# Optimization experiments

Hardware: AMD Instinct MI355X
Metric: run time of the kernel (lower is better)

Reference implementation:

```python
import jax, jax.numpy as jnp
import numpy as np
from jax import lax


def conv2d(x, w, pad):
    return lax.conv_general_dilated(x, w, (1, 1), [(pad, pad), (pad, pad)],
                                    dimension_numbers=('NCHW', 'OIHW', 'NCHW'))


def deform_conv2d(x, offset, w, b, k, pad):
    # torchvision-style DeformConv2d, stride 1, dilation 1, 1 group.
    # offset: [B, 2*k*k, H, W], pairs ordered (dy, dx) per kernel tap (row-major).
    B, C, H, W = x.shape
    KK = k * k
    off = offset.reshape(B, KK, 2, H, W)
    ky, kx = jnp.meshgrid(jnp.arange(k), jnp.arange(k), indexing='ij')
    ky = ky.reshape(1, KK, 1, 1).astype(x.dtype)
    kx = kx.reshape(1, KK, 1, 1).astype(x.dtype)
    gy = jnp.arange(H, dtype=x.dtype).reshape(1, 1, H, 1)
    gx = jnp.arange(W, dtype=x.dtype).reshape(1, 1, 1, W)
    ys = gy + ky - pad + off[:, :, 0]  # [B, KK, H, W]
    xs = gx + kx - pad + off[:, :, 1]
    y0 = jnp.floor(ys)
    x0 = jnp.floor(xs)
    y1 = y0 + 1.0
    x1 = x0 + 1.0
    img = x.reshape(B, C, H * W)

    def corner(yc, xc, wt):
        # zero padding outside the image
        valid = (yc >= 0) & (yc <= H - 1) & (xc >= 0) & (xc <= W - 1)
        idx = (jnp.clip(yc, 0, H - 1) * W + jnp.clip(xc, 0, W - 1)).astype(jnp.int32).reshape(B, -1)
        g = jax.vmap(lambda im, ix: jnp.take(im, ix, axis=1))(img, idx)  # [B, C, KK*H*W]
        return g.reshape(B, C, KK, H, W) * (wt * valid)[:, None]

    v = (corner(y0, x0, (y1 - ys) * (x1 - xs))
         + corner(y0, x1, (y1 - ys) * (xs - x0))
         + corner(y1, x0, (ys - y0) * (x1 - xs))
         + corner(y1, x1, (ys - y0) * (xs - x0)))  # [B, C, KK, H, W]
    out = jnp.einsum('bckhw,ock->bohw', v, w.reshape(w.shape[0], C, KK))
    return out + b[None, :, None, None]


def setup_inputs() -> dict:
    key = jax.random.key(0)
    ks = jax.random.split(key, 16)
    f32 = jnp.float32
    dim = 64

    def rn(k, shape, s):
        return jax.random.normal(k, shape, f32) * s

    return {
        'x': rn(ks[0], (4, dim, 96, 96), 1.0),
        'w_off3': rn(ks[1], (18, dim, 3, 3), 0.01), 'b_off3': jnp.zeros((18,), f32),
        'w_off5': rn(ks[2], (50, dim, 3, 3), 0.01), 'b_off5': jnp.zeros((50,), f32),
        'w_off7': rn(ks[3], (98, dim, 3, 3), 0.01), 'b_off7': jnp.zeros((98,), f32),
        'w_d3': rn(ks[4], (dim, dim, 3, 3), 0.04), 'b_d3': rn(ks[5], (dim,), 0.01),
        'w_d5': rn(ks[6], (dim, dim, 5, 5), 0.025), 'b_d5': rn(ks[7], (dim,), 0.01),
        'w_d7': rn(ks[8], (dim, dim, 7, 7), 0.018), 'b_d7': rn(ks[9], (dim,), 0.01),
        'w_sp': rn(ks[10], (1, 2, 7, 7), 0.1),
        'w_ca1': rn(ks[11], (12, 3 * dim, 1, 1), 0.07),
        'w_ca2': rn(ks[12], (3 * dim, 12, 1, 1), 0.28),
    }


def reference(x, w_off3, b_off3, w_off5, b_off5, w_off7, b_off7,
              w_d3, b_d3, w_d5, b_d5, w_d7, b_d7, w_sp, w_ca1, w_ca2):
    off3 = conv2d(x, w_off3, 1) + b_off3[None, :, None, None]
    off5 = conv2d(x, w_off5, 1) + b_off5[None, :, None, None]
    off7 = conv2d(x, w_off7, 1) + b_off7[None, :, None, None]
    a1 = deform_conv2d(x, off3, w_d3, b_d3, 3, 1)
    a2 = deform_conv2d(x, off5, w_d5, b_d5, 5, 2)
    a3 = deform_conv2d(x, off7, w_d7, b_d7, 7, 3)
    res = jnp.concatenate([a1, a2, a3], axis=1)  # [B, 3C, H, W]

    # SpatialAttention: channel mean/max -> 7x7 conv -> sigmoid
    sp_in = jnp.concatenate([jnp.mean(res, axis=1, keepdims=True),
                             jnp.max(res, axis=1, keepdims=True)], axis=1)
    sp = jax.nn.sigmoid(conv2d(sp_in, w_sp, 3))  # [B, 1, H, W]

    # ChannelAttention: shared MLP on avg- and max-pooled descriptors
    def fc(t):
        return conv2d(jnp.maximum(conv2d(t, w_ca1, 0), 0.0), w_ca2, 0)

    avg = jnp.mean(res, axis=(2, 3), keepdims=True)
    mx = jnp.max(res, axis=(2, 3), keepdims=True)
    ch = jax.nn.sigmoid(fc(avg) + fc(mx))  # [B, 3C, 1, 1]

    C = x.shape[1]
    c1, c2, c3 = ch[:, :C], ch[:, C:2 * C], ch[:, 2 * C:]
    return a1 * (sp + c1) + a2 * (sp + c2) + a3 * (sp + c3)
```

## Files before the change

kernel.cpp:

```cpp
#include <hip/hip_runtime.h>
#include <math.h>

#define H 96
#define W 96
#define HW (H*W)
#define CIN 64
#define NB 4
#define NOFF 166
#define OFFROW 168
#define HWP (HW+1)

typedef __attribute__((ext_vector_type(8)))  short short8;
typedef __attribute__((ext_vector_type(8)))  _Float16 half8;
typedef __attribute__((ext_vector_type(16))) float f32x16;
typedef unsigned short ushort_t;

static const size_t OFF_ALL = 0;
static const size_t RES     = OFF_ALL + (size_t)NB*HW*OFFROW;
static const size_t XB16    = RES + (size_t)NB*192*HW;
static const size_t WTD3    = XB16 + (size_t)NB*64*HWP/2;
static const size_t WTD5    = WTD3 + 9*4096/2;
static const size_t WTD7    = WTD5 + 25*4096/2;
static const size_t WOFF    = WTD7 + 49*4096/2;
static const size_t BOFF    = WOFF + 9*192*64/2;
static const size_t SPIN    = BOFF + 192;
static const size_t SPATT   = SPIN + (size_t)NB*2*HW;
static const size_t POOLAVG = SPATT + (size_t)NB*HW;
static const size_t POOLMAX = POOLAVG + NB*192;
static const size_t CHATT   = POOLMAX + NB*192;

__device__ __forceinline__ ushort_t f2h(float f) {
    _Float16 h = (_Float16)f;
    return __builtin_bit_cast(unsigned short, h);
}
__device__ __forceinline__ half8 as_h8(short8 s) {
    return __builtin_bit_cast(half8, s);
}
__device__ __forceinline__ half8 splat8(float f) {
    _Float16 h = (_Float16)f;
    half8 v;
    #pragma unroll
    for (int j = 0; j < 8; j++) v[j] = h;
    return v;
}

__global__ __launch_bounds__(256) void prep_kernel(
    const float* __restrict__ x, ushort_t* __restrict__ xb,
    const float* __restrict__ w3, const float* __restrict__ w5,
    const float* __restrict__ w7,
    const float* __restrict__ ob3, const float* __restrict__ ob5,
    const float* __restrict__ ob7,
    const float* __restrict__ ow3, const float* __restrict__ ow5,
    const float* __restrict__ ow7,
    ushort_t* __restrict__ wt3, ushort_t* __restrict__ wt5,
    ushort_t* __restrict__ wt7,
    ushort_t* __restrict__ woff, float* __restrict__ boff)
{
    const int bid = blockIdx.x;
    const int t = threadIdx.x;
    if (bid < 576) {
        __shared__ ushort_t tile[64][66];
        int b = bid / 144;
        int p0 = (bid % 144) * 64;
        int q = t >> 6, ln = t & 63;
        #pragma unroll
        for (int i = 0; i < 16; i++) {
            int c = q * 16 + i;
            tile[ln][c] = f2h(x[((size_t)(b * 64 + c)) * HW + p0 + ln]);
        }
        if (p0 == 0 && t < 64) xb[((size_t)b * HWP + HW) * 64 + t] = 0;
        __syncthreads();
        #pragma unroll
        for (int i = 0; i < 16; i++) {
            int pos = q * 16 + i;
            xb[((size_t)b * HWP + p0 + pos) * 64 + ln] = tile[pos][ln];
        }
        return;
    }
    int idx = (bid - 576) * 256 + t;
    if (idx < 83 * 4096) {
        const float* src; ushort_t* dst; int KK; int o;
        if (idx < 9 * 4096)       { src = w3; dst = wt3; KK = 9;  o = idx; }
        else if (idx < 34 * 4096) { src = w5; dst = wt5; KK = 25; o = idx - 9 * 4096; }
        else                      { src = w7; dst = wt7; KK = 49; o = idx - 34 * 4096; }
        int j    = o & 7;
        int l31  = (o >> 3) & 31;
        int lh   = (o >> 8) & 1;
        int cs   = (o >> 9) & 3;
        int half = (o >> 11) & 1;
        int kk   = o >> 12;
        int co = half * 32 + l31;
        int c  = cs * 16 + lh * 8 + j;
        dst[o] = f2h(src[((size_t)co * 64 + c) * KK + kk]);
        return;
    }
    int o = idx - 83 * 4096;
    if (o >= 9 * 192 * 64) return;
    int c  = o & 63;
    int co = (o >> 6) % 192;
    int kk = o / (192 * 64);
    float v = 0.f;
    if (co < 18)       v = ow3[(co * 64 + c) * 9 + kk];
    else if (co < 68)  v = ow5[((co - 18) * 64 + c) * 9 + kk];
    else if (co < 166) v = ow7[((co - 68) * 64 + c) * 9 + kk];
    woff[(kk * 192 + co) * 64 + c] = f2h(v);
    if (kk == 0 && c == 0) {
        float bv = 0.f;
        if (co < 18)       bv = ob3[co];
        else if (co < 68)  bv = ob5[co - 18];
        else if (co < 166) bv = ob7[co - 68];
        boff[co] = bv;
    }
}

__global__ __launch_bounds__(256, 3) void offset_mfma_kernel(
    const ushort_t* __restrict__ xb,
    const ushort_t* __restrict__ woff,
    const float* __restrict__ bias_all,
    float* __restrict__ off_all)
{
    __shared__ float red[6144];
    const int t = threadIdx.x;
    const int lane = t & 63, l31 = lane & 31, lh = lane >> 5;
    const int wave = t >> 6;
    const int mhalf = wave >> 1, khalf = wave & 1;
    const int xcd = blockIdx.x & 7, u = blockIdx.x >> 3;
    const int b = xcd >> 1;
    const int v = u * 2 + (xcd & 1);
    const int npos = v * 32 + l31;
    const int h = npos / 96, w = npos % 96;
    const int c0 = 8 * lh;
    const ushort_t* xbase = xb + (size_t)b * HWP * 64;

    f32x16 acc0, acc1, acc2;
    #pragma unroll
    for (int r = 0; r < 16; r++) { acc0[r] = 0.f; acc1[r] = 0.f; acc2[r] = 0.f; }

    const int kk0 = khalf ? 5 : 0, kk1 = khalf ? 9 : 5;
    const int mt0 = mhalf * 3;
    for (int kk = kk0; kk < kk1; kk++) {
        int ky = kk / 3, kx = kk % 3;
        int y = h + ky - 1, x = w + kx - 1;
        bool ok = ((unsigned)y < (unsigned)H) && ((unsigned)x < (unsigned)W);
        int o = ok ? (y * W + x) : HW;
        const ushort_t* px = xbase + (size_t)o * 64 + c0;
        const ushort_t* wk = woff + (size_t)kk * 12288;
        #pragma unroll
        for (int cs = 0; cs < 4; cs++) {
            int cc = cs * 16;
            half8 bfrag = as_h8(*(const short8*)(px + cc));
            half8 a0 = as_h8(*(const short8*)(wk + (size_t)((mt0 + 0) * 32 + l31) * 64 + cc + c0));
            half8 a1 = as_h8(*(const short8*)(wk + (size_t)((mt0 + 1) * 32 + l31) * 64 + cc + c0));
            half8 a2 = as_h8(*(const short8*)(wk + (size_t)((mt0 + 2) * 32 + l31) * 64 + cc + c0));
            acc0 = __builtin_amdgcn_mfma_f32_32x32x16_f16(a0, bfrag, acc0, 0, 0, 0);
            acc1 = __builtin_amdgcn_mfma_f32_32x32x16_f16(a1, bfrag, acc1, 0, 0, 0);
            acc2 = __builtin_amdgcn_mfma_f32_32x32x16_f16(a2, bfrag, acc2, 0, 0, 0);
        }
    }

    if (khalf) {
        float* rp = red + mhalf * 3072;
        #pragma unroll
        for (int r = 0; r < 16; r++) {
            rp[(0 * 16 + r) * 64 + lane] = acc0[r];
            rp[(1 * 16 + r) * 64 + lane] = acc1[r];
            rp[(2 * 16 + r) * 64 + lane] = acc2[r];
        }
    }
    __syncthreads();
    if (!khalf) {
        const float* rp = red + mhalf * 3072;
        #pragma unroll
        for (int r = 0; r < 16; r++) {
            acc0[r] += rp[(0 * 16 + r) * 64 + lane];
            acc1[r] += rp[(1 * 16 + r) * 64 + lane];
            acc2[r] += rp[(2 * 16 + r) * 64 + lane];
        }
        float* row = off_all + ((size_t)b * HW + npos) * OFFROW;
        #pragma unroll
        for (int m = 0; m < 3; m++) {
            const f32x16& a = (m == 0) ? acc0 : (m == 1) ? acc1 : acc2;
            int mt = mt0 + m;
            #pragma unroll
            for (int q = 0; q < 4; q++) {
                int base = mt * 32 + 8 * q + 4 * lh;
                if (base < 166) {
                    float4 vv = make_float4(a[4 * q + 0] + bias_all[base + 0],
                                            a[4 * q + 1] + bias_all[base + 1],
                                            a[4 * q + 2] + bias_all[base + 2],
                                            a[4 * q + 3] + bias_all[base + 3]);
                    *(float4*)(row + base) = vv;
                }
            }
        }
    }
}

__device__ __forceinline__ void store_tile_stats(int b, int tile, int lane, int g,
                                                 const float* __restrict__ bias,
                                                 const f32x16& acc0, const f32x16& acc1,
                                                 float* __restrict__ res,
                                                 float& psum, float& pmax)
{
    const int l31 = lane & 31, lh = lane >> 5;
    const int npos = tile * 32 + l31;
    size_t rb = (((size_t)b * 3 + g) * 64) * HW + npos;
    #pragma unroll
    for (int r = 0; r < 16; r++) {
        int co = (r & 3) + 8 * (r >> 2) + 4 * lh;
        float v0 = acc0[r] + bias[co];
        float v1 = acc1[r] + bias[co + 32];
        res[rb + (size_t)co * HW]        = v0;
        res[rb + (size_t)(co + 32) * HW] = v1;
        psum += v0 + v1;
        pmax = fmaxf(pmax, fmaxf(v0, v1));
    }
}

#define MG  5
#define PNY 12
#define PNX 43
#define PXS 144
#define PRS (PNX * PXS)

template<int K, int PAD>
__device__ __forceinline__ void deform_span(
    const float* __restrict__ offp, const ushort_t* __restrict__ wtf,
    int kk0, int kk1, int h, int w, int w0, int l31, int lh,
    const char* lds, f32x16& acc0, f32x16& acc1)
{
    const int lh16 = lh * 16;
    const float2* offp2 = (const float2*)offp;
    float2 off = offp2[kk0];
    for (int kk = kk0; kk < kk1; kk++) {
        float2 noff = offp2[(kk + 1 < kk1) ? kk + 1 : kk];

        int ky = kk / K, kx = kk % K;
        float ys = (float)(h + ky - PAD) + off.x;
        float xs = (float)(w + kx - PAD) + off.y;
        float y0f = floorf(ys), x0f = floorf(xs);
        float fy = ys - y0f, fx = xs - x0f;
        int iy0 = (int)y0f, ix0 = (int)x0f;
        int iy1 = iy0 + 1, ix1 = ix0 + 1;
        float oky0 = ((unsigned)iy0 < (unsigned)H) ? 1.f : 0.f;
        float oky1 = ((unsigned)iy1 < (unsigned)H) ? 1.f : 0.f;
        float okx0 = ((unsigned)ix0 < (unsigned)W) ? 1.f : 0.f;
        float okx1 = ((unsigned)ix1 < (unsigned)W) ? 1.f : 0.f;
        float w00 = (1.f - fy) * (1.f - fx) * oky0 * okx0;
        float w01 = (1.f - fy) * fx * oky0 * okx1;
        float w10 = fy * (1.f - fx) * oky1 * okx0;
        float w11 = fy * fx * oky1 * okx1;
        int cy0 = min(max(iy0, 0), H - 1), cy1 = min(max(iy1, 0), H - 1);
        int cx0 = min(max(ix0, 0), W - 1), cx1 = min(max(ix1, 0), W - 1);
        int r0 = min(max(cy0 - h + MG, 0), PNY - 1);
        int r1 = min(max(cy1 - h + MG, 0), PNY - 1);
        int p0 = min(max(cx0 - w0 + MG, 0), PNX - 1);
        int p1 = min(max(cx1 - w0 + MG, 0), PNX - 1);
        const char* b00 = lds + r0 * PRS + p0 * PXS + lh16;
        const char* b01 = lds + r0 * PRS + p1 * PXS + lh16;
        const char* b10 = lds + r1 * PRS + p0 * PXS + lh16;
        const char* b11 = lds + r1 * PRS + p1 * PXS + lh16;

        half8 W00 = splat8(w00), W01 = splat8(w01);
        half8 W10 = splat8(w10), W11 = splat8(w11);
        const ushort_t* wkf = wtf + (size_t)kk * 4096;
        #pragma unroll
        for (int cs = 0; cs < 4; cs++) {
            half8 q00 = *(const half8*)(b00 + cs * 32);
            half8 q01 = *(const half8*)(b01 + cs * 32);
            half8 q10 = *(const half8*)(b10 + cs * 32);
            half8 q11 = *(const half8*)(b11 + cs * 32);
            half8 bfrag = q00 * W00 + q01 * W01 + q10 * W10 + q11 * W11;
            half8 a0 = as_h8(*(const short8*)(wkf + (size_t)(((0 * 4 + cs) * 2 + lh) * 32 + l31) * 8));
            half8 a1 = as_h8(*(const short8*)(wkf + (size_t)(((1 * 4 + cs) * 2 + lh) * 32 + l31) * 8));
            acc0 = __builtin_amdgcn_mfma_f32_32x32x16_f16(a0, bfrag, acc0, 0, 0, 0);
            acc1 = __builtin_amdgcn_mfma_f32_32x32x16_f16(a1, bfrag, acc1, 0, 0, 0);
        }
        off = noff;
    }
}

__global__ __launch_bounds__(256, 2) void deform_fused_kernel(
    const ushort_t* __restrict__ xb, const float* __restrict__ off_all,
    const ushort_t* __restrict__ wt3, const ushort_t* __restrict__ wt5,
    const ushort_t* __restrict__ wt7,
    const float* __restrict__ b3, const float* __restrict__ b5,
    const float* __restrict__ b7,
    float* __restrict__ res, float* __restrict__ spin)
{
    __shared__ __align__(16) char lds[PNY * PNX * PXS];
    const int t = threadIdx.x;
    const int wave = t >> 6, lane = t & 63;
    const int xcd = blockIdx.x & 7, u = blockIdx.x >> 3;
    const int b = xcd >> 1;
    const int tile = u * 2 + (xcd & 1);

    const int l31 = lane & 31, lh = lane >> 5;
    const int h  = tile / 3;
    const int w0 = (tile % 3) * 32;
    const int w  = w0 + l31;
    const int npos = h * 96 + w;

    const ushort_t* xsrc = xb + (size_t)b * HWP * 64;
    constexpr int NCH = PNY * PNX * 8;
    constexpr int NITER = (NCH + 255) / 256;
    #pragma unroll
    for (int it = 0; it < NITER; it++) {
        int c = t + it * 256;
        if (c < NCH) {
            int rr  = c / (PNX * 8);
            int rem = c - rr * (PNX * 8);
            int pp  = rem >> 3, sub = rem & 7;
            int cy = min(max(h - MG + rr, 0), H - 1);
            int cx = min(max(w0 - MG + pp, 0), W - 1);
            *(float4*)(lds + rr * PRS + pp * PXS + sub * 16) =
                *(const float4*)(xsrc + ((size_t)(cy * W + cx)) * 64 + sub * 8);
        }
    }
    __syncthreads();

    const float* offrow = off_all + ((size_t)b * HW + npos) * OFFROW;

    f32x16 a0A, a1A, a0B, a1B;
    #pragma unroll
    for (int r = 0; r < 16; r++) { a0A[r] = 0.f; a1A[r] = 0.f; a0B[r] = 0.f; a1B[r] = 0.f; }

    if (wave == 0) {
        deform_span<3, 1>(offrow + 0,  wt3, 0, 9,  h, w, w0, l31, lh, lds, a0A, a1A);
        deform_span<5, 2>(offrow + 18, wt5, 0, 12, h, w, w0, l31, lh, lds, a0B, a1B);
    } else if (wave == 1) {
        deform_span<5, 2>(offrow + 18, wt5, 12, 25, h, w, w0, l31, lh, lds, a0A, a1A);
        deform_span<7, 3>(offrow + 68, wt7, 0, 8,   h, w, w0, l31, lh, lds, a0B, a1B);
    } else if (wave == 2) {
        deform_span<7, 3>(offrow + 68, wt7, 8, 29,  h, w, w0, l31, lh, lds, a0A, a1A);
    } else {
        deform_span<7, 3>(offrow + 68, wt7, 29, 49, h, w, w0, l31, lh, lds, a0A, a1A);
    }

    __syncthreads();
    float* slots = (float*)lds;
    if (wave == 1) {
        float* s0 = slots;
        float* s1 = slots + 2048;
        #pragma unroll
        for (int r = 0; r < 16; r++) {
            s0[r * 64 + lane]        = a0A[r];
            s0[(16 + r) * 64 + lane] = a1A[r];
            s1[r * 64 + lane]        = a0B[r];
            s1[(16 + r) * 64 + lane] = a1B[r];
        }
    } else if (wave == 3) {
        float* s2 = slots + 4096;
        #pragma unroll
        for (int r = 0; r < 16; r++) {
            s2[r * 64 + lane]        = a0A[r];
            s2[(16 + r) * 64 + lane] = a1A[r];
        }
    }
    __syncthreads();
    float psum = 0.f, pmax = -3.402823466e+38f;
    if (wave == 0) {
        store_tile_stats(b, tile, lane, 0, b3, a0A, a1A, res, psum, pmax);
        const float* s0 = slots;
        #pragma unroll
        for (int r = 0; r < 16; r++) {
            a0B[r] += s0[r * 64 + lane];
            a1B[r] += s0[(16 + r) * 64 + lane];
        }
        store_tile_stats(b, tile, lane, 1, b5, a0B, a1B, res, psum, pmax);
    } else if (wave == 2) {
        const float* s1 = slots + 2048;
        const float* s2 = slots + 4096;
        #pragma unroll
        for (int r = 0; r < 16; r++) {
            a0A[r] += s1[r * 64 + lane] + s2[r * 64 + lane];
            a1A[r] += s1[(16 + r) * 64 + lane] + s2[(16 + r) * 64 + lane];
        }
        store_tile_stats(b, tile, lane, 2, b7, a0A, a1A, res, psum, pmax);
    }
    if (wave == 0 || wave == 2) {
        psum += __shfl_xor(psum, 32);
        pmax = fmaxf(pmax, __shfl_xor(pmax, 32));
        if (lane < 32) {
            float* pr = (float*)lds + 8192 + (wave == 2 ? 64 : 0);
            pr[lane * 2]     = psum;
            pr[lane * 2 + 1] = pmax;
        }
    }
    __syncthreads();
    if (wave == 1 && lane < 32) {
        const float* pr = (const float*)lds + 8192;
        float s = pr[lane * 2]     + pr[64 + lane * 2];
        float m = fmaxf(pr[lane * 2 + 1], pr[64 + lane * 2 + 1]);
        int np = tile * 32 + lane;
        spin[(size_t)b * 2 * HW + np]      = s * (1.f / 192.f);
        spin[(size_t)b * 2 * HW + HW + np] = m;
    }
}

__global__ __launch_bounds__(256) void pool_kernel(const float* __restrict__ res,
                                                   float* __restrict__ avg,
                                                   float* __restrict__ mx) {
    int bc = blockIdx.x;
    const float* r = res + (size_t)bc * HW;
    int t = threadIdx.x;
    float s = 0.f, m = -3.402823466e+38f;
    for (int i = t; i < HW; i += 256) {
        float v = r[i];
        s += v;
        m = fmaxf(m, v);
    }
    #pragma unroll
    for (int off = 32; off > 0; off >>= 1) {
        s += __shfl_down(s, off);
        m = fmaxf(m, __shfl_down(m, off));
    }
    __shared__ float ss[4], sm[4];
    int wid = t >> 6;
    if ((t & 63) == 0) { ss[wid] = s; sm[wid] = m; }
    __syncthreads();
    if (t == 0) {
        s = ss[0] + ss[1] + ss[2] + ss[3];
        m = fmaxf(fmaxf(sm[0], sm[1]), fmaxf(sm[2], sm[3]));
        avg[bc] = s * (1.f / (float)HW);
        mx[bc]  = m;
    }
}

__global__ __launch_bounds__(256) void att_kernel(
    const float* __restrict__ spin, const float* __restrict__ w_sp,
    float* __restrict__ sp,
    const float* __restrict__ avg, const float* __restrict__ mx,
    const float* __restrict__ w1, const float* __restrict__ w2,
    float* __restrict__ ch)
{
    const int bid = blockIdx.x;
    const int t = threadIdx.x;
    if (bid < 576) {
        int gt  = bid * 256 + t;
        int idx = gt >> 2;
        int q   = gt & 3;
        int w = idx % W;
        int h = (idx / W) % H;
        int b = idx / HW;
        int ci  = q >> 1;
        int dy0 = (q & 1) ? 4 : 0;
        int dy1 = (q & 1) ? 7 : 4;
        const float* pin = spin + ((size_t)b * 2 + ci) * HW;
        const float* wp  = w_sp + ci * 49;
        float acc = 0.f;
        for (int dy = dy0; dy < dy1; dy++) {
            int yy = h + dy - 3;
            if (yy < 0 || yy >= H) continue;
            #pragma unroll
            for (int dx = 0; dx < 7; dx++) {
                int xx = w + dx - 3;
                if (xx < 0 || xx >= W) continue;
                acc = fmaf(pin[yy * W + xx], wp[dy * 7 + dx], acc);
            }
        }
        acc += __shfl_xor(acc, 1);
        acc += __shfl_xor(acc, 2);
        if (q == 0) sp[idx] = 1.f / (1.f + expf(-acc));
        return;
    }
    int b = bid - 576;
    __shared__ float sa[192], sm_[192], h1a[12], h1m[12];
    if (t < 192) { sa[t] = avg[b * 192 + t]; sm_[t] = mx[b * 192 + t]; }
    __syncthreads();
    if (t < 192) {
        int j = t >> 4, lg = t & 15;
        float s1 = 0.f, s2 = 0.f;
        #pragma unroll
        for (int i = 0; i < 12; i++) {
            int c = lg + i * 16;
            float wv = w1[j * 192 + c];
            s1 = fmaf(wv, sa[c], s1);
            s2 = fmaf(wv, sm_[c], s2);
        }
        #pragma unroll
        for (int d = 1; d < 16; d <<= 1) {
            s1 += __shfl_xor(s1, d);
            s2 += __shfl_xor(s2, d);
        }
        if (lg == 0) {
            h1a[j] = fmaxf(s1, 0.f);
            h1m[j] = fmaxf(s2, 0.f);
        }
    }
    __syncthreads();
    if (t < 192) {
        float s = 0.f;
        #pragma unroll
        for (int j = 0; j < 12; j++)
            s = fmaf(w2[t * 12 + j], h1a[j] + h1m[j], s);
        ch[b * 192 + t] = 1.f / (1.f + expf(-s));
    }
}

__global__ void final_kernel(const float* __restrict__ res,
                             const float* __restrict__ sp,
                             const float* __restrict__ ch,
                             float* __restrict__ out) {
    int idx = blockIdx.x * 256 + threadIdx.x;
    int hw4 = idx % (HW / 4);
    int co  = (idx / (HW / 4)) % 64;
    int b   = idx / (64 * (HW / 4));
    size_t rb = (size_t)b * 192 * HW + (size_t)co * HW + hw4 * 4;
    float4 a1 = *(const float4*)(res + rb);
    float4 a2 = *(const float4*)(res + rb + (size_t)64 * HW);
    float4 a3 = *(const float4*)(res + rb + (size_t)128 * HW);
    float4 spv = *(const float4*)(sp + (size_t)b * HW + hw4 * 4);
    float c1 = ch[b * 192 + co];
    float c2 = ch[b * 192 + 64 + co];
    float c3 = ch[b * 192 + 128 + co];
    float4 o;
    o.x = a1.x * (spv.x + c1) + a2.x * (spv.x + c2) + a3.x * (spv.x + c3);
    o.y = a1.y * (spv.y + c1) + a2.y * (spv.y + c2) + a3.y * (spv.y + c3);
    o.z = a1.z * (spv.z + c1) + a2.z * (spv.z + c2) + a3.z * (spv.z + c3);
    o.w = a1.w * (spv.w + c1) + a2.w * (spv.w + c2) + a3.w * (spv.w + c3);
    *(float4*)(out + ((size_t)b * 64 + co) * HW + hw4 * 4) = o;
}

extern "C" void kernel_launch(void* const* d_in, const int* in_sizes, int n_in,
                              void* d_out, int out_size, void* d_ws, size_t ws_size,
                              hipStream_t stream) {
    const float* x      = (const float*)d_in[0];
    const float* w_off3 = (const float*)d_in[1];
    const float* b_off3 = (const float*)d_in[2];
    const float* w_off5 = (const float*)d_in[3];
    const float* b_off5 = (const float*)d_in[4];
    const float* w_off7 = (const float*)d_in[5];
    const float* b_off7 = (const float*)d_in[6];
    const float* w_d3   = (const float*)d_in[7];
    const float* b_d3   = (const float*)d_in[8];
    const float* w_d5   = (const float*)d_in[9];
    const float* b_d5   = (const float*)d_in[10];
    const float* w_d7   = (const float*)d_in[11];
    const float* b_d7   = (const float*)d_in[12];
    const float* w_sp   = (const float*)d_in[13];
    const float* w_ca1  = (const float*)d_in[14];
    const float* w_ca2  = (const float*)d_in[15];

    float* ws = (float*)d_ws;
    float* off_all = ws + OFF_ALL;
    float* res     = ws + RES;
    ushort_t* xb16 = (ushort_t*)(ws + XB16);
    ushort_t* wt3  = (ushort_t*)(ws + WTD3);
    ushort_t* wt5  = (ushort_t*)(ws + WTD5);
    ushort_t* wt7  = (ushort_t*)(ws + WTD7);
    ushort_t* woff = (ushort_t*)(ws + WOFF);
    float* boff = ws + BOFF;
    float* spin = ws + SPIN;
    float* sp   = ws + SPATT;
    float* avgp = ws + POOLAVG;
    float* mxp  = ws + POOLMAX;
    float* chp  = ws + CHATT;

    prep_kernel<<<2336, 256, 0, stream>>>(x, xb16, w_d3, w_d5, w_d7,
                                          b_off3, b_off5, b_off7,
                                          w_off3, w_off5, w_off7,
                                          wt3, wt5, wt7, woff, boff);

    offset_mfma_kernel<<<1152, 256, 0, stream>>>(xb16, woff, boff, off_all);

    deform_fused_kernel<<<1152, 256, 0, stream>>>(xb16, off_all, wt3, wt5, wt7,
                                                  b_d3, b_d5, b_d7, res, spin);

    pool_kernel<<<768, 256, 0, stream>>>(res, avgp, mxp);
    att_kernel<<<580, 256, 0, stream>>>(spin, w_sp, sp, avgp, mxp,
                                        w_ca1, w_ca2, chp);

    final_kernel<<<2304, 256, 0, stream>>>(res, sp, chp, (float*)d_out);
}
```

Baseline: 146.3 us.

## Fuse channel pooling into deform kernel epilogue via atomics, drop pool kernel

Removes the separate pool_kernel that re-read the whole 192-channel result tensor to compute per-channel mean and max. The deform kernel epilogue now reduces each channel across its 32-position tile with cross-lane shuffles and atomically accumulates sums and order-preserving encoded maxima into global buffers, which an extra prep block zeroes. This saves one launch and a full read of res, but adds many shuffles and atomics per tile to the deform epilogue and makes the float sum order nondeterministic.

New measurement: 225.4 us. 1.54x slower.

```diff
diff --git a/kernel.cpp b/kernel.cpp
--- a/kernel.cpp
+++ b/kernel.cpp
@@ -25,8 +25,8 @@
 static const size_t BOFF    = WOFF + 9*192*64/2;
 static const size_t SPIN    = BOFF + 192;
 static const size_t SPATT   = SPIN + (size_t)NB*2*HW;
-static const size_t POOLAVG = SPATT + (size_t)NB*HW;
-static const size_t POOLMAX = POOLAVG + NB*192;
+static const size_t POOLSUM = SPATT + (size_t)NB*HW;
+static const size_t POOLMAX = POOLSUM + NB*192;
 static const size_t CHATT   = POOLMAX + NB*192;
 
 __device__ __forceinline__ ushort_t f2h(float f) {
@@ -42,6 +42,15 @@
     #pragma unroll
     for (int j = 0; j < 8; j++) v[j] = h;
     return v;
+}
+
+__device__ __forceinline__ unsigned fenc(float f) {
+    unsigned u = __float_as_uint(f);
+    return (u & 0x80000000u) ? ~u : (u | 0x80000000u);
+}
+__device__ __forceinline__ float fdec(unsigned k) {
+    return (k & 0x80000000u) ? __uint_as_float(k ^ 0x80000000u)
+                             : __uint_as_float(~k);
 }
 
 __global__ __launch_bounds__(256) void prep_kernel(
@@ -54,10 +63,18 @@
     const float* __restrict__ ow7,
     ushort_t* __restrict__ wt3, ushort_t* __restrict__ wt5,
     ushort_t* __restrict__ wt7,
-    ushort_t* __restrict__ woff, float* __restrict__ boff)
+    ushort_t* __restrict__ woff, float* __restrict__ boff,
+    float* __restrict__ sumb, unsigned* __restrict__ maxb)
 {
     const int bid = blockIdx.x;
     const int t = threadIdx.x;
+    if (bid == 2336) {
+        for (int i = t; i < NB * 192; i += 256) {
+            sumb[i] = 0.f;
+            maxb[i] = 0u;
+        }
+        return;
+    }
     if (bid < 576) {
         __shared__ ushort_t tile[64][66];
         int b = bid / 144;
@@ -200,7 +217,9 @@
                                                  const float* __restrict__ bias,
                                                  const f32x16& acc0, const f32x16& acc1,
                                                  float* __restrict__ res,
-                                                 float& psum, float& pmax)
+                                                 float& psum, float& pmax,
+                                                 float* __restrict__ sumb,
+                                                 unsigned* __restrict__ maxb)
 {
     const int l31 = lane & 31, lh = lane >> 5;
     const int npos = tile * 32 + l31;
@@ -214,6 +233,20 @@
         res[rb + (size_t)(co + 32) * HW] = v1;
         psum += v0 + v1;
         pmax = fmaxf(pmax, fmaxf(v0, v1));
+        float s0 = v0, s1 = v1, m0 = v0, m1 = v1;
+        #pragma unroll
+        for (int d = 1; d < 32; d <<= 1) {
+            s0 += __shfl_xor(s0, d);
+            s1 += __shfl_xor(s1, d);
+            m0 = fmaxf(m0, __shfl_xor(m0, d));
+            m1 = fmaxf(m1, __shfl_xor(m1, d));
+        }
+        if (l31 == co) {
+            atomicAdd(&sumb[co], s0);
+            atomicAdd(&sumb[co + 32], s1);
+            atomicMax(&maxb[co], fenc(m0));
+            atomicMax(&maxb[co + 32], fenc(m1));
+        }
     }
 }
 
@@ -286,7 +319,8 @@
     const ushort_t* __restrict__ wt7,
     const float* __restrict__ b3, const float* __restrict__ b5,
     const float* __restrict__ b7,
-    float* __restrict__ res, float* __restrict__ spin)
+    float* __restrict__ res, float* __restrict__ spin,
+    float* __restrict__ sumb, unsigned* __restrict__ maxb)
 {
     __shared__ __align__(16) char lds[PNY * PNX * PXS];
     const int t = threadIdx.x;
@@ -360,14 +394,16 @@
     __syncthreads();
     float psum = 0.f, pmax = -3.402823466e+38f;
     if (wave == 0) {
-        store_tile_stats(b, tile, lane, 0, b3, a0A, a1A, res, psum, pmax);
+        store_tile_stats(b, tile, lane, 0, b3, a0A, a1A, res, psum, pmax,
+                         sumb + b * 192 + 0, maxb + b * 192 + 0);
         const float* s0 = slots;
         #pragma unroll
         for (int r = 0; r < 16; r++) {
             a0B[r] += s0[r * 64 + lane];
             a1B[r] += s0[(16 + r) * 64 + lane];
         }
-        store_tile_stats(b, tile, lane, 1, b5, a0B, a1B, res, psum, pmax);
+        store_tile_stats(b, tile, lane, 1, b5, a0B, a1B, res, psum, pmax,
+                         sumb + b * 192 + 64, maxb + b * 192 + 64);
     } else if (wave == 2) {
         const float* s1 = slots + 2048;
         const float* s2 = slots + 4096;
@@ -376,7 +412,8 @@
             a0A[r] += s1[r * 64 + lane] + s2[r * 64 + lane];
             a1A[r] += s1[(16 + r) * 64 + lane] + s2[(16 + r) * 64 + lane];
         }
-        store_tile_stats(b, tile, lane, 2, b7, a0A, a1A, res, psum, pmax);
+        store_tile_stats(b, tile, lane, 2, b7, a0A, a1A, res, psum, pmax,
+                         sumb + b * 192 + 128, maxb + b * 192 + 128);
     }
     if (wave == 0 || wave == 2) {
         psum += __shfl_xor(psum, 32);
@@ -398,39 +435,10 @@
     }
 }
 
-__global__ __launch_bounds__(256) void pool_kernel(const float* __restrict__ res,
-                                                   float* __restrict__ avg,
-                                                   float* __restrict__ mx) {
-    int bc = blockIdx.x;
-    const float* r = res + (size_t)bc * HW;
-    int t = threadIdx.x;
-    float s = 0.f, m = -3.402823466e+38f;
-    for (int i = t; i < HW; i += 256) {
-        float v = r[i];
-        s += v;
-        m = fmaxf(m, v);
-    }
-    #pragma unroll
-    for (int off = 32; off > 0; off >>= 1) {
-        s += __shfl_down(s, off);
-        m = fmaxf(m, __shfl_down(m, off));
-    }
-    __shared__ float ss[4], sm[4];
-    int wid = t >> 6;
-    if ((t & 63) == 0) { ss[wid] = s; sm[wid] = m; }
-    __syncthreads();
-    if (t == 0) {
-        s = ss[0] + ss[1] + ss[2] + ss[3];
-        m = fmaxf(fmaxf(sm[0], sm[1]), fmaxf(sm[2], sm[3]));
-        avg[bc] = s * (1.f / (float)HW);
-        mx[bc]  = m;
-    }
-}
-
 __global__ __launch_bounds__(256) void att_kernel(
     const float* __restrict__ spin, const float* __restrict__ w_sp,
     float* __restrict__ sp,
-    const float* __restrict__ avg, const float* __restrict__ mx,
+    const float* __restrict__ sumb, const unsigned* __restrict__ maxb,
     const float* __restrict__ w1, const float* __restrict__ w2,
     float* __restrict__ ch)
 {
@@ -466,7 +474,10 @@
     }
     int b = bid - 576;
     __shared__ float sa[192], sm_[192], h1a[12], h1m[12];
-    if (t < 192) { sa[t] = avg[b * 192 + t]; sm_[t] = mx[b * 192 + t]; }
+    if (t < 192) {
+        sa[t]  = sumb[b * 192 + t] * (1.f / (float)HW);
+        sm_[t] = fdec(maxb[b * 192 + t]);
+    }
     __syncthreads();
     if (t < 192) {
         int j = t >> 4, lg = t & 15;
@@ -553,22 +564,23 @@
     float* boff = ws + BOFF;
     float* spin = ws + SPIN;
     float* sp   = ws + SPATT;
-    float* avgp = ws + POOLAVG;
-    float* mxp  = ws + POOLMAX;
+    float* sumb = ws + POOLSUM;
+    unsigned* maxb = (unsigned*)(ws + POOLMAX);
     float* chp  = ws + CHATT;
 
-    prep_kernel<<<2336, 256, 0, stream>>>(x, xb16, w_d3, w_d5, w_d7,
+    prep_kernel<<<2337, 256, 0, stream>>>(x, xb16, w_d3, w_d5, w_d7,
                                           b_off3, b_off5, b_off7,
                                           w_off3, w_off5, w_off7,
-                                          wt3, wt5, wt7, woff, boff);
+                                          wt3, wt5, wt7, woff, boff,
+                                          sumb, maxb);
 
     offset_mfma_kernel<<<1152, 256, 0, stream>>>(xb16, woff, boff, off_all);
 
     deform_fused_kernel<<<1152, 256, 0, stream>>>(xb16, off_all, wt3, wt5, wt7,
-                                                  b_d3, b_d5, b_d7, res, spin);
-
-    pool_kernel<<<768, 256, 0, stream>>>(res, avgp, mxp);
-    att_kernel<<<580, 256, 0, stream>>>(spin, w_sp, sp, avgp, mxp,
+                                                  b_d3, b_d5, b_d7, res, spin,
+                                                  sumb, maxb);
+
+    att_kernel<<<580, 256, 0, stream>>>(spin, w_sp, sp, sumb, maxb,
                                         w_ca1, w_ca2, chp);
 
     final_kernel<<<2304, 256, 0, stream>>>(res, sp, chp, (float*)d_out);
```
